# Kernel tuning notes

Hardware: AMD Instinct MI355X
Metric: run time of the kernel (lower is better)

Reference implementation:

```python
import jax, jax.numpy as jnp
import numpy as np

B, N, D_IN, D_PROJ, C = 1024, 50000, 768, 128, 100
BW2 = float(D_PROJ)   # RBF bandwidth^2
EPS = 1e-10


def setup_inputs() -> dict:
    key = jax.random.key(0)
    ks = jax.random.split(key, 6)
    x = jax.random.normal(ks[0], (B, D_IN), jnp.float32)
    X = jax.random.normal(ks[1], (N, D_IN), jnp.float32)
    # learned projection (Linear D_IN -> D_PROJ); scale keeps projected coords ~N(0,1)
    Wp = jax.random.normal(ks[2], (D_IN, D_PROJ), jnp.float32) * (D_IN ** -0.5)
    bp = jnp.zeros((D_PROJ,), jnp.float32)
    Y = jax.random.randint(ks[3], (N,), 0, C, jnp.int32)
    SorP_train = jax.random.normal(ks[4], (N, C), jnp.float32)
    SorP_q = jax.random.normal(ks[5], (B, C), jnp.float32)
    return dict(x=x, X=X, Wp=Wp, bp=bp, Y=Y, SorP_train=SorP_train, SorP_q=SorP_q)


def _perm_locs(SorP):
    # locs = argsort(argsort(SorP, descending)) per row
    sort_idx = jnp.argsort(-SorP, axis=-1)
    return jnp.argsort(sort_idx, axis=-1)


def reference(x, X, Wp, bp, Y, SorP_train, SorP_q):
    px = x @ Wp + bp            # [B, D_PROJ]
    pX = X @ Wp + bp            # [N, D_PROJ]
    # squared euclidean distances via GEMM
    sqd = ((px * px).sum(-1, keepdims=True)
           + (pX * pX).sum(-1)[None, :]
           - 2.0 * (px @ pX.T))                     # [B, N]
    Kis = jnp.exp(-sqd / (2.0 * BW2))               # RBF kernel, self-sim == 1
    # drop_self: zero out (near-)self matches
    Kis = jnp.where(Kis < 1.0 - EPS, Kis, 0.0)
    # rows with ~zero total mass -> uniform eps
    Kis = jnp.where(Kis.sum(1, keepdims=True) > EPS, Kis, EPS)
    # MODE_SORT label encoding: one_hot(locs_train[i, Y[i]])
    locs_t = _perm_locs(SorP_train)                 # [N, C]
    Y1h = jax.nn.one_hot(locs_t[jnp.arange(N), Y], C, dtype=jnp.float32)
    pred = Kis @ Y1h                                # [B, C]
    pred = pred / pred.sum(1, keepdims=True)
    # per-sample reorder (vectorized gather instead of the python loop)
    locs_q = _perm_locs(SorP_q)                     # [B, C]
    return jnp.take_along_axis(pred, locs_q, axis=1)
```

## Files before the change

### kernel.cpp

```cpp
#include <hip/hip_runtime.h>


typedef short  bf8v  __attribute__((ext_vector_type(8)));
typedef float  f32x4 __attribute__((ext_vector_type(4)));

#define NTRAIN 50000
#define NPAD   50048
#define NTILES 391
#define BQ     1024
#define DIN    768
#define DP     128
#define NCLS   100
#define PSTRIDE 104
#define PCOLS  104
#define FIXS   2097152.0f
#define FIXI   (1.0f / 2097152.0f)

__device__ __forceinline__ short f2bf(float x) {
    unsigned u = __float_as_uint(x);
    u += 0x7FFFu + ((u >> 16) & 1u);
    return (short)(u >> 16);
}

#define AS1U(p) ((const __attribute__((address_space(1))) unsigned int*)(unsigned long long)(p))
#define AS3U(p) ((__attribute__((address_space(3))) unsigned int*)(unsigned int)(unsigned long long)(p))

__global__ __launch_bounds__(256) void k_prep(const float* __restrict__ Wp,
                                              short* __restrict__ WpP,
                                              const float* __restrict__ S,
                                              const int* __restrict__ Y,
                                              int* __restrict__ lab) {
    if (blockIdx.x < 48) {
        int tid = blockIdx.x * 256 + threadIdx.x;
        if (tid >= 24 * 8 * 64) return;
        int l = tid & 63, cb = (tid >> 6) & 7, q = tid >> 9;
        int c = cb * 16 + (l & 15);
        int g = l >> 4;
        bf8v o;
#pragma unroll
        for (int j = 0; j < 8; ++j) {
            int k = q * 32 + g * 8 + j;
            o[j] = f2bf(Wp[k * DP + c]);
        }
        *reinterpret_cast<bf8v*>(WpP + (size_t)tid * 8) = o;
        return;
    }
    int w = threadIdx.x >> 6, l = threadIdx.x & 63;
    int i = (blockIdx.x - 48) * 4 + w;
    if (i >= NPAD) return;
    int cnt = 0;
    if (i < NTRAIN) {
        int y = Y[i];
        float t = S[(size_t)i * NCLS + y];
        float v1 = S[(size_t)i * NCLS + l];
        bool p1 = (v1 > t) || (v1 == t && l < y);
        unsigned long long b1 = __ballot(p1);
        bool p2 = false;
        if (l < NCLS - 64) {
            float v2 = S[(size_t)i * NCLS + 64 + l];
            p2 = (v2 > t) || (v2 == t && (64 + l) < y);
        }
        unsigned long long b2 = __ballot(p2);
        cnt = __popcll(b1) + __popcll(b2);
    }
    if (l == 0) lab[i] = cnt;
}

__global__ __launch_bounds__(256, 3) void k_proj(const float* __restrict__ Xin,
                                                 const short* __restrict__ WpP,
                                                 const float* __restrict__ bp,
                                                 short* __restrict__ outP,
                                                 float* __restrict__ normv,
                                                 int Mreal) {
    __shared__ __align__(16) float Xlds[2][64 * 64];
    const int tid = threadIdx.x;
    const int w = tid >> 6, l = tid & 63, g = l >> 4, li = l & 15;
    const int rowblk = blockIdx.x * 64;

    f32x4 acc[8];
#pragma unroll
    for (int cb = 0; cb < 8; ++cb) acc[cb] = (f32x4){0.f, 0.f, 0.f, 0.f};

#define STAGE64(lbuf, kb)                                                     \
    {                                                                         \
        _Pragma("unroll")                                                     \
        for (int it = 0; it < 4; ++it) {                                      \
            int s  = w * 256 + it * 64 + l;                                   \
            int r  = s >> 4;                                                  \
            int c4 = (s & 15) ^ (r & 7);                                      \
            int rg = rowblk + r;                                              \
            rg = (rg < Mreal) ? rg : (Mreal - 1);                             \
            const float* gp = Xin + (size_t)rg * DIN + (kb) * 64 + c4 * 4;    \
            const float* lp = (lbuf) + (w * 256 + it * 64) * 4;               \
            __builtin_amdgcn_global_load_lds(AS1U(gp), AS3U(lp), 16, 0, 0);   \
        }                                                                     \
    }
#define ISSUE_B(dst, kb)                                                      \
    {                                                                         \
        _Pragma("unroll")                                                     \
        for (int f = 0; f < 16; ++f)                                          \
            dst[f] = *reinterpret_cast<const bf8v*>(                          \
                WpP + ((size_t)((kb) * 16 + f) * 64 + l) * 8);                \
    }
#define READ_A(avec, lbuf)                                                    \
    {                                                                         \
        const float* rbase = (lbuf) + (w * 16 + li) * 64;                     \
        _Pragma("unroll")                                                     \
        for (int kc = 0; kc < 2; ++kc) {                                      \
            int s0 = (kc * 8 + g * 2)     ^ (li & 7);                         \
            int s1 = (kc * 8 + g * 2 + 1) ^ (li & 7);                         \
            avec[kc * 2]     = *reinterpret_cast<const float4*>(rbase + s0 * 4); \
            avec[kc * 2 + 1] = *reinterpret_cast<const float4*>(rbase + s1 * 4); \
        }                                                                     \
    }
#define COMPUTE(breg, avec)                                                   \
    {                                                                         \
        _Pragma("unroll")                                                     \
        for (int kc = 0; kc < 2; ++kc) {                                      \
            float4 a0 = avec[kc * 2], a1 = avec[kc * 2 + 1];                  \
            bf8v af;                                                          \
            af[0] = f2bf(a0.x); af[1] = f2bf(a0.y);                           \
            af[2] = f2bf(a0.z); af[3] = f2bf(a0.w);                           \
            af[4] = f2bf(a1.x); af[5] = f2bf(a1.y);                           \
            af[6] = f2bf(a1.z); af[7] = f2bf(a1.w);                           \
            _Pragma("unroll")                                                 \
            for (int cb = 0; cb < 8; ++cb)                                    \
                acc[cb] = __builtin_amdgcn_mfma_f32_16x16x32_bf16(            \
                              af, breg[kc * 8 + cb], acc[cb], 0, 0, 0);       \
        }                                                                     \
    }

    bf8v breg[16];
    float4 a[4];

    STAGE64(&Xlds[0][0], 0);
    STAGE64(&Xlds[1][0], 1);
    ISSUE_B(breg, 0);

#pragma unroll 1
    for (int kb = 0; kb < 12; ++kb) {
        asm volatile("s_waitcnt vmcnt(20)" ::: "memory");
        READ_A(a, &Xlds[kb & 1][0]);
        asm volatile("s_waitcnt lgkmcnt(0)" ::: "memory");
        __builtin_amdgcn_sched_barrier(0);
        if (kb + 2 < 12) {
            STAGE64(&Xlds[kb & 1][0], kb + 2);
            asm volatile("s_waitcnt vmcnt(4)" ::: "memory");
        } else {
            asm volatile("s_waitcnt vmcnt(0)" ::: "memory");
        }
        __builtin_amdgcn_sched_barrier(0);
        COMPUTE(breg, a);
        if (kb + 1 < 12) ISSUE_B(breg, kb + 1);
    }
#undef STAGE64
#undef ISSUE_B
#undef READ_A
#undef COMPUTE

    float bpv[8];
#pragma unroll
    for (int cb = 0; cb < 8; ++cb) bpv[cb] = bp[cb * 16 + li];
#pragma unroll
    for (int cb = 0; cb < 8; ++cb)
#pragma unroll
        for (int r = 0; r < 4; ++r) acc[cb][r] += bpv[cb];

#pragma unroll
    for (int r = 0; r < 4; ++r) {
        float s = 0.f;
#pragma unroll
        for (int cb = 0; cb < 8; ++cb) {
            float v = acc[cb][r];
            s += v * v;
        }
        s += __shfl_xor(s, 1);
        s += __shfl_xor(s, 2);
        s += __shfl_xor(s, 4);
        s += __shfl_xor(s, 8);
        int grow = rowblk + w * 16 + 4 * g + r;
        if (li == 0) normv[grow] = (grow < Mreal) ? s : 1e30f;
    }

#pragma unroll
    for (int cb = 0; cb < 8; ++cb) {
        int d = cb * 16 + li;
        int q = d >> 5, g2 = (d & 31) >> 3, j = d & 7;
#pragma unroll
        for (int r = 0; r < 4; ++r) {
            int grow = rowblk + w * 16 + 4 * g + r;
            float v = (grow < Mreal) ? acc[cb][r] : 0.f;
            size_t e = ((size_t)((grow >> 4) * 4 + q) * 64 +
                        (g2 * 16 + (grow & 15))) * 8 + j;
            outP[e] = f2bf(v);
        }
    }
}

__global__ __launch_bounds__(256) void k_main(const short* __restrict__ pxp,
                                              const short* __restrict__ pXp,
                                              const float* __restrict__ qn,
                                              const float* __restrict__ kn,
                                              const int* __restrict__ lab,
                                              float* __restrict__ part,
                                              int NCH) {
    __shared__ __align__(16) unsigned plds[128 * PSTRIDE];
    const int tid = threadIdx.x;
    const int w = tid >> 6, l = tid & 63, g = l >> 4, li = l & 15;
    const int ch = blockIdx.x;
    const int bt = blockIdx.y;

    for (int s = tid; s < 128 * PSTRIDE; s += 256) plds[s] = 0u;
    __syncthreads();

    bf8v af[2][4];
#pragma unroll
    for (int rb = 0; rb < 2; ++rb)
#pragma unroll
        for (int q = 0; q < 4; ++q) {
            int RB = bt * 8 + w * 2 + rb;
            af[rb][q] = *reinterpret_cast<const bf8v*>(
                            pxp + (size_t)((RB * 4 + q) * 64 + l) * 8);
        }
    float qnv[2][4];
#pragma unroll
    for (int rb = 0; rb < 2; ++rb)
#pragma unroll
        for (int r = 0; r < 4; ++r)
            qnv[rb][r] = qn[bt * 128 + w * 32 + rb * 16 + 4 * g + r];

#pragma unroll 1
    for (int t = ch; t < NTILES; t += NCH) {
        const int i0 = t * 128;
        float knv8[8];
        int   labv8[8];
#pragma unroll
        for (int ib = 0; ib < 8; ++ib) {
            knv8[ib]  = kn[i0 + ib * 16 + li];
            labv8[ib] = lab[i0 + ib * 16 + li];
        }
        bf8v bfr2[2][4];
        {
            const int RBi = (i0 >> 4);
#pragma unroll
            for (int q = 0; q < 4; ++q)
                bfr2[0][q] = *reinterpret_cast<const bf8v*>(
                                 pXp + (size_t)((RBi * 4 + q) * 64 + l) * 8);
        }
#pragma unroll
        for (int ib = 0; ib < 8; ++ib) {
            if (ib < 7) {
                const int RBn = (i0 >> 4) + ib + 1;
#pragma unroll
                for (int q = 0; q < 4; ++q)
                    bfr2[(ib + 1) & 1][q] = *reinterpret_cast<const bf8v*>(
                        pXp + (size_t)((RBn * 4 + q) * 64 + l) * 8);
            }
            f32x4 s0 = (f32x4){0.f, 0.f, 0.f, 0.f};
            f32x4 s1 = (f32x4){0.f, 0.f, 0.f, 0.f};
#pragma unroll
            for (int q = 0; q < 4; ++q) {
                s0 = __builtin_amdgcn_mfma_f32_16x16x32_bf16(af[0][q], bfr2[ib & 1][q], s0, 0, 0, 0);
                s1 = __builtin_amdgcn_mfma_f32_16x16x32_bf16(af[1][q], bfr2[ib & 1][q], s1, 0, 0, 0);
            }
            const float knv  = knv8[ib];
            const int   labv = labv8[ib];
#pragma unroll
            for (int rb = 0; rb < 2; ++rb) {
                f32x4 sv = rb ? s1 : s0;
#pragma unroll
                for (int r = 0; r < 4; ++r) {
                    float sqd = qnv[rb][r] + knv - 2.f * sv[r];
                    float kis = __expf(sqd * (-1.f / 256.f));
                    kis = (kis < 1.0f) ? kis : 0.f;
                    unsigned qv = (unsigned)__float2uint_rn(kis * FIXS);
                    int rowl = w * 32 + rb * 16 + 4 * g + r;
                    atomicAdd(&plds[rowl * PSTRIDE + labv], qv);
                }
            }
        }
    }

#pragma unroll 1
    for (int rr = 0; rr < 32; ++rr) {
        int row = w * 32 + rr;
        if (l < PCOLS / 2) {
            uint2 u = *reinterpret_cast<const uint2*>(&plds[row * PSTRIDE + l * 2]);
            float2 v = make_float2((float)u.x * FIXI, (float)u.y * FIXI);
            int grow = bt * 128 + row;
            *reinterpret_cast<float2*>(
                &part[((size_t)grow * NCH + ch) * PCOLS + l * 2]) = v;
        }
    }
}

__global__ __launch_bounds__(256) void k_final(const float* __restrict__ part,
                                               const float* __restrict__ SorPq,
                                               float* __restrict__ out,
                                               int NCH) {
    __shared__ float sp[NCLS];
    __shared__ float pr2[2][PCOLS];
    int t = threadIdx.x, b = blockIdx.x;
    int c = t & 127, h = t >> 7;
    if (h == 1 && c < NCLS) sp[c] = SorPq[(size_t)b * NCLS + c];
    if (c < PCOLS) {
        float s = 0.f;
        int half = NCH >> 1;
        const float* p = part + ((size_t)b * NCH + (size_t)h * half) * PCOLS + c;
        for (int ch = 0; ch < half; ++ch) s += p[(size_t)ch * PCOLS];
        pr2[h][c] = s;
    }
    __syncthreads();
    if (t < PCOLS) pr2[0][t] += pr2[1][t];
    __syncthreads();
    if (t < NCLS) {
        float tot = 0.f;
        for (int k = 0; k < NCLS; ++k) tot += pr2[0][k];
        float s = sp[t];
        int r = 0;
        for (int k = 0; k < NCLS; ++k) {
            float sk = sp[k];
            r += (sk > s || (sk == s && k < t)) ? 1 : 0;
        }
        out[(size_t)b * NCLS + t] = pr2[0][r] / tot;
    }
}

extern "C" void kernel_launch(void* const* d_in, const int* in_sizes, int n_in,
                              void* d_out, int out_size, void* d_ws, size_t ws_size,
                              hipStream_t stream) {
    const float* x    = (const float*)d_in[0];
    const float* X    = (const float*)d_in[1];
    const float* Wp   = (const float*)d_in[2];
    const float* bp   = (const float*)d_in[3];
    const int*   Y    = (const int*)  d_in[4];
    const float* SPt  = (const float*)d_in[5];
    const float* SPq  = (const float*)d_in[6];
    float* out = (float*)d_out;

    char* ws = (char*)d_ws;
    short* WpP = (short*)(ws + 0);
    short* pXp = (short*)(ws + 196608);
    short* pxq = (short*)(ws + 13008896);
    float* kn  = (float*)(ws + 13271040);
    float* qn  = (float*)(ws + 13471232);
    int*   lab = (int*)  (ws + 13475328);
    float* part= (float*)(ws + 13675520);

    const size_t base = 13675520;
    const size_t per  = (size_t)BQ * PCOLS * 4;
    int NCH = 96;
    if (ws_size > base) {
        size_t fit = (ws_size - base) / per;
        if ((size_t)NCH > fit) NCH = (int)fit;
    } else {
        NCH = 8;
    }
    NCH &= ~7;
    if (NCH < 8) NCH = 8;

    k_prep<<<48 + (NPAD + 3) / 4, 256, 0, stream>>>(Wp, WpP, SPt, Y, lab);
    k_proj<<<NPAD / 64, 256, 0, stream>>>(X, WpP, bp, pXp, kn, NTRAIN);
    k_proj<<<(BQ + 63) / 64, 256, 0, stream>>>(x, WpP, bp, pxq, qn, BQ);
    k_main<<<dim3(NCH, 8), 256, 0, stream>>>(pxq, pXp, qn, kn, lab, part, NCH);
    k_final<<<BQ, 256, 0, stream>>>(part, SPq, out, NCH);
}
```

Before: 124.3 us.

## Fuse projections and label prep into one launch, deepen B prefetch, shrink LDS stride

Merges the two projection launches and the label-rank computation into a single k_front kernel, leaving only the Wp packing as a separate launch. This cuts launch count and lets the small query projection and the label work overlap with the large train projection. In k_main, the pXp fragment prefetch goes from a 2-deep ring to a 4-deep ring loaded 3 tiles ahead, which adds register pressure. It also shrinks the LDS histogram stride from 104 to 102 to change bank mapping, and trims the final reduction loops to 100 columns. The stride change means the partial writer now copies 102 columns while part still uses 104-column rows, so the last two columns stay unwritten; k_final no longer reads them.

```diff
diff --git a/kernel.cpp b/kernel.cpp
--- a/kernel.cpp
+++ b/kernel.cpp
@@ -11,10 +11,13 @@
 #define DIN    768
 #define DP     128
 #define NCLS   100
-#define PSTRIDE 104
+#define PSTRIDE 102
 #define PCOLS  104
 #define FIXS   2097152.0f
 #define FIXI   (1.0f / 2097152.0f)
+#define NBX    (NPAD / 64)
+#define NBQ    (BQ / 64)
+#define NBL    ((NPAD + 3) / 4)
 
 __device__ __forceinline__ short f2bf(float x) {
     unsigned u = __float_as_uint(x);
@@ -25,57 +28,32 @@
 #define AS1U(p) ((const __attribute__((address_space(1))) unsigned int*)(unsigned long long)(p))
 #define AS3U(p) ((__attribute__((address_space(3))) unsigned int*)(unsigned int)(unsigned long long)(p))
 
-__global__ __launch_bounds__(256) void k_prep(const float* __restrict__ Wp,
-                                              short* __restrict__ WpP,
-                                              const float* __restrict__ S,
-                                              const int* __restrict__ Y,
-                                              int* __restrict__ lab) {
-    if (blockIdx.x < 48) {
-        int tid = blockIdx.x * 256 + threadIdx.x;
-        if (tid >= 24 * 8 * 64) return;
-        int l = tid & 63, cb = (tid >> 6) & 7, q = tid >> 9;
-        int c = cb * 16 + (l & 15);
-        int g = l >> 4;
-        bf8v o;
-#pragma unroll
-        for (int j = 0; j < 8; ++j) {
-            int k = q * 32 + g * 8 + j;
-            o[j] = f2bf(Wp[k * DP + c]);
-        }
-        *reinterpret_cast<bf8v*>(WpP + (size_t)tid * 8) = o;
-        return;
-    }
-    int w = threadIdx.x >> 6, l = threadIdx.x & 63;
-    int i = (blockIdx.x - 48) * 4 + w;
-    if (i >= NPAD) return;
-    int cnt = 0;
-    if (i < NTRAIN) {
-        int y = Y[i];
-        float t = S[(size_t)i * NCLS + y];
-        float v1 = S[(size_t)i * NCLS + l];
-        bool p1 = (v1 > t) || (v1 == t && l < y);
-        unsigned long long b1 = __ballot(p1);
-        bool p2 = false;
-        if (l < NCLS - 64) {
-            float v2 = S[(size_t)i * NCLS + 64 + l];
-            p2 = (v2 > t) || (v2 == t && (64 + l) < y);
-        }
-        unsigned long long b2 = __ballot(p2);
-        cnt = __popcll(b1) + __popcll(b2);
-    }
-    if (l == 0) lab[i] = cnt;
-}
-
-__global__ __launch_bounds__(256, 3) void k_proj(const float* __restrict__ Xin,
-                                                 const short* __restrict__ WpP,
-                                                 const float* __restrict__ bp,
-                                                 short* __restrict__ outP,
-                                                 float* __restrict__ normv,
-                                                 int Mreal) {
-    __shared__ __align__(16) float Xlds[2][64 * 64];
+__global__ __launch_bounds__(256) void k_pack_wp(const float* __restrict__ Wp,
+                                                 short* __restrict__ WpP) {
+    int tid = blockIdx.x * 256 + threadIdx.x;
+    if (tid >= 24 * 8 * 64) return;
+    int l = tid & 63, cb = (tid >> 6) & 7, q = tid >> 9;
+    int c = cb * 16 + (l & 15);
+    int g = l >> 4;
+    bf8v o;
+#pragma unroll
+    for (int j = 0; j < 8; ++j) {
+        int k = q * 32 + g * 8 + j;
+        o[j] = f2bf(Wp[k * DP + c]);
+    }
+    *reinterpret_cast<bf8v*>(WpP + (size_t)tid * 8) = o;
+}
+
+__device__ __forceinline__ void proj_body(const float* __restrict__ Xin,
+                                          const short* __restrict__ WpP,
+                                          const float* __restrict__ bp,
+                                          short* __restrict__ outP,
+                                          float* __restrict__ normv,
+                                          int Mreal, int blk,
+                                          float* __restrict__ Xlds) {
     const int tid = threadIdx.x;
     const int w = tid >> 6, l = tid & 63, g = l >> 4, li = l & 15;
-    const int rowblk = blockIdx.x * 64;
+    const int rowblk = blk * 64;
 
     f32x4 acc[8];
 #pragma unroll
@@ -102,61 +80,54 @@
             dst[f] = *reinterpret_cast<const bf8v*>(                          \
                 WpP + ((size_t)((kb) * 16 + f) * 64 + l) * 8);                \
     }
-#define READ_A(avec, lbuf)                                                    \
-    {                                                                         \
-        const float* rbase = (lbuf) + (w * 16 + li) * 64;                     \
-        _Pragma("unroll")                                                     \
-        for (int kc = 0; kc < 2; ++kc) {                                      \
-            int s0 = (kc * 8 + g * 2)     ^ (li & 7);                         \
-            int s1 = (kc * 8 + g * 2 + 1) ^ (li & 7);                         \
-            avec[kc * 2]     = *reinterpret_cast<const float4*>(rbase + s0 * 4); \
-            avec[kc * 2 + 1] = *reinterpret_cast<const float4*>(rbase + s1 * 4); \
-        }                                                                     \
-    }
-#define COMPUTE(breg, avec)                                                   \
-    {                                                                         \
-        _Pragma("unroll")                                                     \
-        for (int kc = 0; kc < 2; ++kc) {                                      \
-            float4 a0 = avec[kc * 2], a1 = avec[kc * 2 + 1];                  \
-            bf8v af;                                                          \
-            af[0] = f2bf(a0.x); af[1] = f2bf(a0.y);                           \
-            af[2] = f2bf(a0.z); af[3] = f2bf(a0.w);                           \
-            af[4] = f2bf(a1.x); af[5] = f2bf(a1.y);                           \
-            af[6] = f2bf(a1.z); af[7] = f2bf(a1.w);                           \
-            _Pragma("unroll")                                                 \
-            for (int cb = 0; cb < 8; ++cb)                                    \
-                acc[cb] = __builtin_amdgcn_mfma_f32_16x16x32_bf16(            \
-                              af, breg[kc * 8 + cb], acc[cb], 0, 0, 0);       \
-        }                                                                     \
-    }
 
     bf8v breg[16];
     float4 a[4];
 
-    STAGE64(&Xlds[0][0], 0);
-    STAGE64(&Xlds[1][0], 1);
+    STAGE64(Xlds, 0);
+    STAGE64(Xlds + 4096, 1);
     ISSUE_B(breg, 0);
 
 #pragma unroll 1
     for (int kb = 0; kb < 12; ++kb) {
+        float* tb = Xlds + (kb & 1) * 4096;
         asm volatile("s_waitcnt vmcnt(20)" ::: "memory");
-        READ_A(a, &Xlds[kb & 1][0]);
+        {
+            const float* rbase = tb + (w * 16 + li) * 64;
+#pragma unroll
+            for (int kc = 0; kc < 2; ++kc) {
+                int s0 = (kc * 8 + g * 2)     ^ (li & 7);
+                int s1 = (kc * 8 + g * 2 + 1) ^ (li & 7);
+                a[kc * 2]     = *reinterpret_cast<const float4*>(rbase + s0 * 4);
+                a[kc * 2 + 1] = *reinterpret_cast<const float4*>(rbase + s1 * 4);
+            }
+        }
         asm volatile("s_waitcnt lgkmcnt(0)" ::: "memory");
         __builtin_amdgcn_sched_barrier(0);
         if (kb + 2 < 12) {
-            STAGE64(&Xlds[kb & 1][0], kb + 2);
+            STAGE64(tb, kb + 2);
             asm volatile("s_waitcnt vmcnt(4)" ::: "memory");
         } else {
             asm volatile("s_waitcnt vmcnt(0)" ::: "memory");
         }
         __builtin_amdgcn_sched_barrier(0);
-        COMPUTE(breg, a);
+#pragma unroll
+        for (int kc = 0; kc < 2; ++kc) {
+            float4 a0 = a[kc * 2], a1 = a[kc * 2 + 1];
+            bf8v af;
+            af[0] = f2bf(a0.x); af[1] = f2bf(a0.y);
+            af[2] = f2bf(a0.z); af[3] = f2bf(a0.w);
+            af[4] = f2bf(a1.x); af[5] = f2bf(a1.y);
+            af[6] = f2bf(a1.z); af[7] = f2bf(a1.w);
+#pragma unroll
+            for (int cb = 0; cb < 8; ++cb)
+                acc[cb] = __builtin_amdgcn_mfma_f32_16x16x32_bf16(
+                              af, breg[kc * 8 + cb], acc[cb], 0, 0, 0);
+        }
         if (kb + 1 < 12) ISSUE_B(breg, kb + 1);
     }
 #undef STAGE64
 #undef ISSUE_B
-#undef READ_A
-#undef COMPUTE
 
     float bpv[8];
 #pragma unroll
@@ -195,6 +166,48 @@
             outP[e] = f2bf(v);
         }
     }
+}
+
+__global__ __launch_bounds__(256, 3) void k_front(const float* __restrict__ X,
+                                                  const float* __restrict__ x,
+                                                  const short* __restrict__ WpP,
+                                                  const float* __restrict__ bp,
+                                                  short* __restrict__ pXp,
+                                                  short* __restrict__ pxq,
+                                                  float* __restrict__ kn,
+                                                  float* __restrict__ qn,
+                                                  const float* __restrict__ S,
+                                                  const int* __restrict__ Y,
+                                                  int* __restrict__ lab) {
+    __shared__ __align__(16) float Xlds[2 * 64 * 64];
+    int b = blockIdx.x;
+    if (b < NBX) {
+        proj_body(X, WpP, bp, pXp, kn, NTRAIN, b, Xlds);
+        return;
+    }
+    if (b < NBX + NBQ) {
+        proj_body(x, WpP, bp, pxq, qn, BQ, b - NBX, Xlds);
+        return;
+    }
+    int w = threadIdx.x >> 6, l = threadIdx.x & 63;
+    int i = (b - NBX - NBQ) * 4 + w;
+    if (i >= NPAD) return;
+    int cnt = 0;
+    if (i < NTRAIN) {
+        int y = Y[i];
+        float t = S[(size_t)i * NCLS + y];
+        float v1 = S[(size_t)i * NCLS + l];
+        bool p1 = (v1 > t) || (v1 == t && l < y);
+        unsigned long long b1 = __ballot(p1);
+        bool p2 = false;
+        if (l < NCLS - 64) {
+            float v2 = S[(size_t)i * NCLS + 64 + l];
+            p2 = (v2 > t) || (v2 == t && (64 + l) < y);
+        }
+        unsigned long long b2 = __ballot(p2);
+        cnt = __popcll(b1) + __popcll(b2);
+    }
+    if (l == 0) lab[i] = cnt;
 }
 
 __global__ __launch_bounds__(256) void k_main(const short* __restrict__ pxp,
@@ -232,6 +245,7 @@
 #pragma unroll 1
     for (int t = ch; t < NTILES; t += NCH) {
         const int i0 = t * 128;
+        const int RB0 = i0 >> 4;
         float knv8[8];
         int   labv8[8];
 #pragma unroll
@@ -239,29 +253,27 @@
             knv8[ib]  = kn[i0 + ib * 16 + li];
             labv8[ib] = lab[i0 + ib * 16 + li];
         }
-        bf8v bfr2[2][4];
-        {
-            const int RBi = (i0 >> 4);
+        bf8v bfr[4][4];
+#pragma unroll
+        for (int p = 0; p < 3; ++p)
 #pragma unroll
             for (int q = 0; q < 4; ++q)
-                bfr2[0][q] = *reinterpret_cast<const bf8v*>(
-                                 pXp + (size_t)((RBi * 4 + q) * 64 + l) * 8);
-        }
+                bfr[p][q] = *reinterpret_cast<const bf8v*>(
+                    pXp + (size_t)(((RB0 + p) * 4 + q) * 64 + l) * 8);
 #pragma unroll
         for (int ib = 0; ib < 8; ++ib) {
-            if (ib < 7) {
-                const int RBn = (i0 >> 4) + ib + 1;
+            if (ib + 3 < 8) {
 #pragma unroll
                 for (int q = 0; q < 4; ++q)
-                    bfr2[(ib + 1) & 1][q] = *reinterpret_cast<const bf8v*>(
-                        pXp + (size_t)((RBn * 4 + q) * 64 + l) * 8);
+                    bfr[(ib + 3) & 3][q] = *reinterpret_cast<const bf8v*>(
+                        pXp + (size_t)(((RB0 + ib + 3) * 4 + q) * 64 + l) * 8);
             }
             f32x4 s0 = (f32x4){0.f, 0.f, 0.f, 0.f};
             f32x4 s1 = (f32x4){0.f, 0.f, 0.f, 0.f};
 #pragma unroll
             for (int q = 0; q < 4; ++q) {
-                s0 = __builtin_amdgcn_mfma_f32_16x16x32_bf16(af[0][q], bfr2[ib & 1][q], s0, 0, 0, 0);
-                s1 = __builtin_amdgcn_mfma_f32_16x16x32_bf16(af[1][q], bfr2[ib & 1][q], s1, 0, 0, 0);
+                s0 = __builtin_amdgcn_mfma_f32_16x16x32_bf16(af[0][q], bfr[ib & 3][q], s0, 0, 0, 0);
+                s1 = __builtin_amdgcn_mfma_f32_16x16x32_bf16(af[1][q], bfr[ib & 3][q], s1, 0, 0, 0);
             }
             const float knv  = knv8[ib];
             const int   labv = labv8[ib];
@@ -284,7 +296,7 @@
 #pragma unroll 1
     for (int rr = 0; rr < 32; ++rr) {
         int row = w * 32 + rr;
-        if (l < PCOLS / 2) {
+        if (l < PSTRIDE / 2) {
             uint2 u = *reinterpret_cast<const uint2*>(&plds[row * PSTRIDE + l * 2]);
             float2 v = make_float2((float)u.x * FIXI, (float)u.y * FIXI);
             int grow = bt * 128 + row;
@@ -303,7 +315,7 @@
     int t = threadIdx.x, b = blockIdx.x;
     int c = t & 127, h = t >> 7;
     if (h == 1 && c < NCLS) sp[c] = SorPq[(size_t)b * NCLS + c];
-    if (c < PCOLS) {
+    if (c < NCLS) {
         float s = 0.f;
         int half = NCH >> 1;
         const float* p = part + ((size_t)b * NCH + (size_t)h * half) * PCOLS + c;
@@ -311,7 +323,7 @@
         pr2[h][c] = s;
     }
     __syncthreads();
-    if (t < PCOLS) pr2[0][t] += pr2[1][t];
+    if (t < NCLS) pr2[0][t] += pr2[1][t];
     __syncthreads();
     if (t < NCLS) {
         float tot = 0.f;
@@ -359,9 +371,9 @@
     NCH &= ~7;
     if (NCH < 8) NCH = 8;
 
-    k_prep<<<48 + (NPAD + 3) / 4, 256, 0, stream>>>(Wp, WpP, SPt, Y, lab);
-    k_proj<<<NPAD / 64, 256, 0, stream>>>(X, WpP, bp, pXp, kn, NTRAIN);
-    k_proj<<<(BQ + 63) / 64, 256, 0, stream>>>(x, WpP, bp, pxq, qn, BQ);
+    k_pack_wp<<<48, 256, 0, stream>>>(Wp, WpP);
+    k_front<<<NBX + NBQ + NBL, 256, 0, stream>>>(X, x, WpP, bp, pXp, pxq,
+                                                 kn, qn, SPt, Y, lab);
     k_main<<<dim3(NCH, 8), 256, 0, stream>>>(pxq, pXp, qn, kn, lab, part, NCH);
     k_final<<<BQ, 256, 0, stream>>>(part, SPq, out, NCH);
 }
```

After: 111.9 us. -10.0%, faster.
